# Optimization experiments

Hardware: AMD Instinct MI355X
Metric: run time of the kernel (lower is better)

The kernel has to match this reference:

```python
import jax, jax.numpy as jnp
import numpy as np

N_ATOMS = 512
N_SAMPLES = 2 ** 15  # 32768
N_ITER = 64


def time_domain_to_real(x):
    # rfft then concat(real, imag) along last dim -> length 2*(N//2+1)
    s = jnp.fft.rfft(x, axis=-1)
    return jnp.concatenate([s.real, s.imag], axis=-1)


def real_to_time_domain(x):
    half = x.shape[-1] // 2
    c = x[..., :half] + 1j * x[..., half:]
    return jnp.fft.irfft(c, axis=-1)  # n = 2*(half-1) = N_SAMPLES


def setup_inputs() -> dict:
    key = jax.random.key(0)
    k1, k2 = jax.random.split(key)
    x = jax.random.normal(k1, (64, 1, N_SAMPLES), dtype=jnp.float32)
    # learned atoms, initialized exactly as in Model.__init__
    env = jnp.linspace(1.0, 0.0, N_SAMPLES, dtype=jnp.float32) ** 12
    atoms_td = jax.random.uniform(k2, (1, N_ATOMS, N_SAMPLES), dtype=jnp.float32,
                                  minval=-0.01, maxval=0.01) * env[None, None, :]
    atoms = time_domain_to_real(atoms_td)  # (1, N_ATOMS, 32770)
    return {"x": x, "atoms": atoms}


def reference(x, atoms):
    xr = time_domain_to_real(x)            # (B, 1, L), L = 32770
    an = atoms / jnp.linalg.norm(atoms, axis=-1, keepdims=True)  # unit_norm over last axis
    an = an[0]                             # (A, L)
    res0 = xr[:, 0, :]                     # (B, L)
    rec0 = jnp.zeros_like(res0)

    def step(carry, _):
        res, rec = carry
        # sum(atoms * residual, -1) == dot products -> avoid (B,A,L) intermediate
        dots = jnp.einsum('bl,al->ba', res, an)      # (B, A)
        idx = jnp.argmax(dots, axis=1)               # (B,)
        best = an[idx] * res                         # take_along_dim(corr) == atoms[idx]*res
        return (res - best, rec + best), None

    (res, rec), _ = jax.lax.scan(step, (res0, rec0), None, length=N_ITER)
    reconstruction = real_to_time_domain(rec[:, None, :])  # (B, 1, N_SAMPLES)
    return reconstruction, res[:, None, :]
```

## Files before the change

kernel.cpp:

```cpp
#include <hip/hip_runtime.h>
#include <math.h>

#define NSAMP 32768
#define MH    16384
#define LFREQ 32770
#define NRE   16385
#define NB    64
#define NA    512
#define NITER 64
#define RSTR  32772

#define KPS    33280
#define NSL    64
#define USLICE 8
#define NCH    4097

typedef __attribute__((ext_vector_type(8))) short bf16x8;
typedef __attribute__((ext_vector_type(8))) unsigned short u16x8;
typedef __attribute__((ext_vector_type(4))) float f32x4;

__device__ __forceinline__ int rev4_14(int v) {
  unsigned r = __brev((unsigned)v) >> 18;
  r = ((r & 0x1555u) << 1) | ((r >> 1) & 0x1555u);
  return (int)r;
}

__device__ __forceinline__ unsigned short f2bf(float f) {
  unsigned u = __float_as_uint(f);
  u = (u + 0x7fffu + ((u >> 16) & 1u)) >> 16;
  return (unsigned short)u;
}
__device__ __forceinline__ float bf2f(unsigned short h) {
  return __uint_as_float(((unsigned)h) << 16);
}

__device__ __forceinline__ float2 cmul(float2 a, float2 b) {
  return make_float2(a.x * b.x - a.y * b.y, a.x * b.y + a.y * b.x);
}

__global__ __launch_bounds__(1024) void fft_fwd_kernel(const float* __restrict__ x,
                                                       float* __restrict__ res0,
                                                       unsigned short* __restrict__ resH,
                                                       unsigned short* __restrict__ resL) {
  extern __shared__ float2 s[];
  const int b = blockIdx.x, t = threadIdx.x;
  const float2* xrow = (const float2*)(x + (size_t)b * NSAMP);
  for (int m = t; m < MH; m += 1024) s[m] = xrow[rev4_14(m)];
  __syncthreads();
  for (int st = 0; st < 7; ++st) {
    const int q = 1 << (2 * st);
    const float fac = 6.283185307179586f / (float)(4 * q);
    for (int j = t; j < MH / 4; j += 1024) {
      const int blk = j >> (2 * st), pos = j & (q - 1);
      const int i0 = (blk << (2 * st + 2)) + pos;
      float sn, cs; __sincosf(fac * (float)pos, &sn, &cs);
      const float2 w1 = make_float2(cs, -sn);
      const float2 w2 = cmul(w1, w1);
      const float2 w3 = cmul(w2, w1);
      const float2 a0 = s[i0], a1 = s[i0 + q], a2 = s[i0 + 2 * q], a3 = s[i0 + 3 * q];
      const float2 x1 = cmul(w1, a1), x2 = cmul(w2, a2), x3 = cmul(w3, a3);
      const float2 s0 = make_float2(a0.x + x2.x, a0.y + x2.y);
      const float2 s1 = make_float2(a0.x - x2.x, a0.y - x2.y);
      const float2 t0 = make_float2(x1.x + x3.x, x1.y + x3.y);
      const float2 t1 = make_float2(x1.x - x3.x, x1.y - x3.y);
      s[i0]         = make_float2(s0.x + t0.x, s0.y + t0.y);
      s[i0 + q]     = make_float2(s1.x + t1.y, s1.y - t1.x);
      s[i0 + 2 * q] = make_float2(s0.x - t0.x, s0.y - t0.y);
      s[i0 + 3 * q] = make_float2(s1.x - t1.y, s1.y + t1.x);
    }
    __syncthreads();
  }
  float* rr = res0 + (size_t)b * RSTR;
  unsigned short* hrow = resH + (size_t)b * KPS;
  unsigned short* lrow = resL + (size_t)b * KPS;
  const float fac2 = 6.283185307179586f / (float)NSAMP;
  for (int k = t; k < MH; k += 1024) {
    if (k == 0) {
      const float2 z0 = s[0];
      const float dc = z0.x + z0.y, ny = z0.x - z0.y;
      rr[0] = dc;   rr[NRE] = 0.f;
      rr[MH] = ny;  rr[NRE + MH] = 0.f;
      unsigned short h;
      h = f2bf(dc); hrow[0] = h;  lrow[0] = f2bf(dc - bf2f(h));
      h = f2bf(ny); hrow[MH] = h; lrow[MH] = f2bf(ny - bf2f(h));
      hrow[NRE] = 0; lrow[NRE] = 0;
      hrow[NRE + MH] = 0; lrow[NRE + MH] = 0;
    } else {
      const float2 zk = s[k], zm = s[MH - k];
      const float xer = 0.5f * (zk.x + zm.x), xei = 0.5f * (zk.y - zm.y);
      const float p = 0.5f * (zk.y + zm.y);
      const float q = -0.5f * (zk.x - zm.x);
      float sn, cs; __sincosf(fac2 * (float)k, &sn, &cs);
      const float vr = xer + cs * p + sn * q;
      const float vi = xei + cs * q - sn * p;
      rr[k]       = vr;
      rr[NRE + k] = vi;
      unsigned short h;
      h = f2bf(vr); hrow[k] = h;       lrow[k] = f2bf(vr - bf2f(h));
      h = f2bf(vi); hrow[NRE + k] = h; lrow[NRE + k] = f2bf(vi - bf2f(h));
    }
  }
}

__global__ __launch_bounds__(1024) void fft_inv_kernel(const float* __restrict__ rec,
                                                       float* __restrict__ out) {
  extern __shared__ float2 s[];
  const int b = blockIdx.x, t = threadIdx.x;
  const float* rr = rec + (size_t)b * RSTR;
  const float fac2 = 6.283185307179586f / (float)NSAMP;
  for (int m = t; m < MH; m += 1024) {
    const int k = rev4_14(m);
    float2 z;
    if (k == 0) {
      const float a0 = rr[0], aM = rr[MH];
      z = make_float2(0.5f * (a0 + aM), 0.5f * (a0 - aM));
    } else {
      const float xr_ = rr[k],       xi_ = rr[NRE + k];
      const float mr  = rr[MH - k],  mi  = rr[NRE + MH - k];
      const float xer = 0.5f * (xr_ + mr), xei = 0.5f * (xi_ - mi);
      const float er  = 0.5f * (xr_ - mr), ei  = 0.5f * (xi_ + mi);
      float sn, cs; __sincosf(fac2 * (float)k, &sn, &cs);
      const float xor_ = cs * er - sn * ei;
      const float xoi  = cs * ei + sn * er;
      z = make_float2(xer - xoi, xei + xor_);
    }
    s[m] = z;
  }
  __syncthreads();
  for (int st = 0; st < 7; ++st) {
    const int q = 1 << (2 * st);
    const float fac = 6.283185307179586f / (float)(4 * q);
    for (int j = t; j < MH / 4; j += 1024) {
      const int blk = j >> (2 * st), pos = j & (q - 1);
      const int i0 = (blk << (2 * st + 2)) + pos;
      float sn, cs; __sincosf(fac * (float)pos, &sn, &cs);
      const float2 w1 = make_float2(cs, sn);
      const float2 w2 = cmul(w1, w1);
      const float2 w3 = cmul(w2, w1);
      const float2 a0 = s[i0], a1 = s[i0 + q], a2 = s[i0 + 2 * q], a3 = s[i0 + 3 * q];
      const float2 x1 = cmul(w1, a1), x2 = cmul(w2, a2), x3 = cmul(w3, a3);
      const float2 s0 = make_float2(a0.x + x2.x, a0.y + x2.y);
      const float2 s1 = make_float2(a0.x - x2.x, a0.y - x2.y);
      const float2 t0 = make_float2(x1.x + x3.x, x1.y + x3.y);
      const float2 t1 = make_float2(x1.x - x3.x, x1.y - x3.y);
      s[i0]         = make_float2(s0.x + t0.x, s0.y + t0.y);
      s[i0 + q]     = make_float2(s1.x - t1.y, s1.y + t1.x);
      s[i0 + 2 * q] = make_float2(s0.x - t0.x, s0.y - t0.y);
      s[i0 + 3 * q] = make_float2(s1.x + t1.y, s1.y - t1.x);
    }
    __syncthreads();
  }
  const float inv = 1.0f / (float)MH;
  float2* orow = (float2*)(out + (size_t)b * NSAMP);
  for (int m = t; m < MH; m += 1024) {
    const float2 z = s[m];
    orow[m] = make_float2(z.x * inv, z.y * inv);
  }
}

__global__ __launch_bounds__(256) void atom_norm_kernel(const float* __restrict__ atoms,
                                                        float* __restrict__ rnorm,
                                                        float* __restrict__ anv) {
  const int a = blockIdx.x, t = threadIdx.x;
  const float2* row2 = (const float2*)(atoms + (size_t)a * LFREQ);
  float ss = 0.f;
  for (int i = t; i < LFREQ / 2; i += 256) {
    const float2 v = row2[i];
    ss += v.x * v.x + v.y * v.y;
  }
  __shared__ float red[256];
  red[t] = ss; __syncthreads();
  for (int st = 128; st > 0; st >>= 1) {
    if (t < st) red[t] += red[t + st];
    __syncthreads();
  }
  if (t == 0) {
    const float rn = 1.0f / sqrtf(red[0]);
    rnorm[a] = rn;
    anv[a] = atoms[(size_t)a * LFREQ + 32768] * rn;
  }
}

__global__ __launch_bounds__(256) void an_bf16_kernel(const float* __restrict__ atoms,
                                                      const float* __restrict__ rnorm,
                                                      unsigned short* __restrict__ anH,
                                                      unsigned short* __restrict__ anL) {
  const int quarter = blockIdx.x;
  const int a = blockIdx.y;
  const int t = threadIdx.x;
  const float rn = rnorm[a];
  const float* row = atoms + (size_t)a * LFREQ;
  unsigned short* hrow = anH + (size_t)a * KPS;
  unsigned short* lrow = anL + (size_t)a * KPS;
  const int c0 = quarter * 1040;
  const int c1 = min(c0 + 1040, KPS / 8);
  for (int c = c0 + t; c < c1; c += 256) {
    const int k0 = c * 8;
    float v[8];
    if (k0 + 8 <= LFREQ) {
      #pragma unroll
      for (int e = 0; e < 4; ++e) {
        const float2 p = *(const float2*)(row + k0 + 2 * e);
        v[2 * e] = p.x; v[2 * e + 1] = p.y;
      }
    } else {
      #pragma unroll
      for (int e = 0; e < 8; ++e) v[e] = (k0 + e < LFREQ) ? row[k0 + e] : 0.f;
    }
    u16x8 hv, lv;
    #pragma unroll
    for (int e = 0; e < 8; ++e) {
      const float sv = v[e] * rn;
      const unsigned short h = f2bf(sv);
      hv[e] = h;
      lv[e] = f2bf(sv - bf2f(h));
    }
    *(u16x8*)(hrow + k0) = hv;
    *(u16x8*)(lrow + k0) = lv;
  }
}

__global__ __launch_bounds__(256) void dots_mfma_kernel(const unsigned short* __restrict__ resH,
                                                        const unsigned short* __restrict__ resL,
                                                        const unsigned short* __restrict__ anH,
                                                        const unsigned short* __restrict__ anL,
                                                        float* __restrict__ partials) {
  __shared__ char smem[65536];
  const int slice = blockIdx.x;
  const int atile = blockIdx.y;
  const int t = threadIdx.x;
  const int w = t >> 6, l = t & 63;
  const int bh = w >> 1, ah = w & 1;
  const int kc0 = slice * 512;

  const unsigned short* gtab = (w == 0) ? resH : (w == 1) ? resL : (w == 2) ? anH : anL;
  const int rowoff = (w >= 2) ? atile * 64 : 0;
  const int lrow = rowoff + (l & 15);
  const int lkof = (l >> 4) * 8;

  f32x4 acc00 = {0.f,0.f,0.f,0.f}, acc01 = acc00, acc10 = acc00, acc11 = acc00;

#define STAGE(cc, bb)                                                                     \
  {                                                                                       \
    const int kc = kc0 + (cc) * 64;                                                       \
    _Pragma("unroll")                                                                     \
    for (int si = 0; si < 8; ++si) {                                                      \
      const unsigned short* g = gtab + (size_t)(lrow + (si >> 1) * 16) * KPS              \
                                + kc + (si & 1) * 32 + lkof;                              \
      char* d = smem + (bb) * 32768 + w * 8192 + si * 1024;                               \
      __builtin_amdgcn_global_load_lds((const __attribute__((address_space(1))) void*)g,  \
                                       (__attribute__((address_space(3))) void*)d,        \
                                       16, 0, 0);                                         \
    }                                                                                     \
  }

#define COMPUTE(bb)                                                                      \
  {                                                                                       \
    const char* base = smem + (bb) * 32768;                                               \
    _Pragma("unroll")                                                                     \
    for (int kk = 0; kk < 2; ++kk) {                                                      \
      const bf16x8 aH0 = *(const bf16x8*)(base + ((bh * 2 + 0) * 2 + kk) * 1024 + l * 16);\
      const bf16x8 aH1 = *(const bf16x8*)(base + ((bh * 2 + 1) * 2 + kk) * 1024 + l * 16);\
      const bf16x8 aL0 = *(const bf16x8*)(base + 8192 + ((bh * 2 + 0) * 2 + kk) * 1024 + l * 16);\
      const bf16x8 aL1 = *(const bf16x8*)(base + 8192 + ((bh * 2 + 1) * 2 + kk) * 1024 + l * 16);\
      const bf16x8 bH0 = *(const bf16x8*)(base + 16384 + ((ah * 2 + 0) * 2 + kk) * 1024 + l * 16);\
      const bf16x8 bH1 = *(const bf16x8*)(base + 16384 + ((ah * 2 + 1) * 2 + kk) * 1024 + l * 16);\
      const bf16x8 bL0 = *(const bf16x8*)(base + 24576 + ((ah * 2 + 0) * 2 + kk) * 1024 + l * 16);\
      const bf16x8 bL1 = *(const bf16x8*)(base + 24576 + ((ah * 2 + 1) * 2 + kk) * 1024 + l * 16);\
      acc00 = __builtin_amdgcn_mfma_f32_16x16x32_bf16(aH0, bH0, acc00, 0, 0, 0);          \
      acc01 = __builtin_amdgcn_mfma_f32_16x16x32_bf16(aH0, bH1, acc01, 0, 0, 0);          \
      acc10 = __builtin_amdgcn_mfma_f32_16x16x32_bf16(aH1, bH0, acc10, 0, 0, 0);          \
      acc11 = __builtin_amdgcn_mfma_f32_16x16x32_bf16(aH1, bH1, acc11, 0, 0, 0);          \
      acc00 = __builtin_amdgcn_mfma_f32_16x16x32_bf16(aH0, bL0, acc00, 0, 0, 0);          \
      acc01 = __builtin_amdgcn_mfma_f32_16x16x32_bf16(aH0, bL1, acc01, 0, 0, 0);          \
      acc10 = __builtin_amdgcn_mfma_f32_16x16x32_bf16(aH1, bL0, acc10, 0, 0, 0);          \
      acc11 = __builtin_amdgcn_mfma_f32_16x16x32_bf16(aH1, bL1, acc11, 0, 0, 0);          \
      acc00 = __builtin_amdgcn_mfma_f32_16x16x32_bf16(aL0, bH0, acc00, 0, 0, 0);          \
      acc01 = __builtin_amdgcn_mfma_f32_16x16x32_bf16(aL0, bH1, acc01, 0, 0, 0);          \
      acc10 = __builtin_amdgcn_mfma_f32_16x16x32_bf16(aL1, bH0, acc10, 0, 0, 0);          \
      acc11 = __builtin_amdgcn_mfma_f32_16x16x32_bf16(aL1, bH1, acc11, 0, 0, 0);          \
    }                                                                                     \
  }

  STAGE(0, 0);
  #pragma unroll
  for (int c = 0; c < 8; ++c) {
    const int buf = c & 1;
    if (c < 7) {
      STAGE(c + 1, buf ^ 1);
      asm volatile("s_waitcnt vmcnt(8)" ::: "memory");
    } else {
      asm volatile("s_waitcnt vmcnt(0)" ::: "memory");
    }
    __builtin_amdgcn_s_barrier();
    __builtin_amdgcn_sched_barrier(0);
    COMPUTE(buf);
    __builtin_amdgcn_sched_barrier(0);
    __builtin_amdgcn_s_barrier();
  }
#undef STAGE
#undef COMPUTE

  const int brow = bh * 32 + (l >> 4) * 4;
  const int acol = atile * 64 + ah * 32 + (l & 15);
  float* pp = partials + ((size_t)brow * NSL + slice) * NA + acol;
  const size_t bstr = (size_t)NSL * NA;
  #pragma unroll
  for (int e = 0; e < 4; ++e) {
    pp[(size_t)e * bstr]             = acc00[e];
    pp[(size_t)e * bstr + 16]        = acc01[e];
    pp[(size_t)(16 + e) * bstr]      = acc10[e];
    pp[(size_t)(16 + e) * bstr + 16] = acc11[e];
  }
}

__global__ __launch_bounds__(256) void reduce_argmax_kernel(const float* __restrict__ partials,
                                                            const unsigned short* __restrict__ resH,
                                                            const unsigned short* __restrict__ resL,
                                                            const float* __restrict__ anv,
                                                            int* __restrict__ bestidx) {
  const int b = blockIdx.x, t = threadIdx.x;
  const float* pb = partials + (size_t)b * NSL * NA;
  float d0 = 0.f, d1 = 0.f;
  #pragma unroll 16
  for (int s = 0; s < NSL; ++s) {
    d0 += pb[(size_t)s * NA + t];
    d1 += pb[(size_t)s * NA + t + 256];
  }
  const float rv = bf2f(resH[(size_t)b * KPS + 32768]) +
                   bf2f(resL[(size_t)b * KPS + 32768]);
  d0 = fmaf(rv, anv[t], d0);
  d1 = fmaf(rv, anv[t + 256], d1);
  float best = d0; int bi = t;
  if (d1 > best) { best = d1; bi = t + 256; }
  __shared__ float sv[256]; __shared__ int si[256];
  sv[t] = best; si[t] = bi; __syncthreads();
  for (int st = 128; st > 0; st >>= 1) {
    if (t < st) {
      const float v2 = sv[t + st]; const int i2 = si[t + st];
      if (v2 > sv[t] || (v2 == sv[t] && i2 < si[t])) { sv[t] = v2; si[t] = i2; }
    }
    __syncthreads();
  }
  if (t == 0) bestidx[b] = si[0];
}

__global__ __launch_bounds__(256) void update_kernel(const float* __restrict__ atoms,
                                                     const float* __restrict__ rnorm,
                                                     const int* __restrict__ bestidx,
                                                     unsigned short* __restrict__ resH,
                                                     unsigned short* __restrict__ resL,
                                                     const float* __restrict__ res0,
                                                     float* __restrict__ rec,
                                                     float* __restrict__ out2,
                                                     int final_out) {
  const int slice = blockIdx.x;
  const int b = blockIdx.y;
  const int t = threadIdx.x;
  const int idx = bestidx[b];
  const float rn = rnorm[idx];
  const float* arow = atoms + (size_t)idx * LFREQ;
  unsigned short* hrow = resH + (size_t)b * KPS;
  unsigned short* lrow = resL + (size_t)b * KPS;
  const float* r0row = res0 + (size_t)b * RSTR;
  float* recrow = rec + (size_t)b * RSTR;
  float* orow = out2 + (size_t)b * LFREQ;
  const int c0 = slice * 513;
  const int c1 = min(c0 + 513, NCH);
  for (int c = c0 + t; c < c1; c += 256) {
    const int k0 = c * 8;
    if (k0 + 8 <= LFREQ) {
      const u16x8 hv0 = *(const u16x8*)(hrow + k0);
      const u16x8 lv0 = *(const u16x8*)(lrow + k0);
      float av[8];
      #pragma unroll
      for (int e = 0; e < 4; ++e) {
        const float2 p = *(const float2*)(arow + k0 + 2 * e);
        av[2 * e] = p.x; av[2 * e + 1] = p.y;
      }
      float nv[8];
      u16x8 hv, lv;
      #pragma unroll
      for (int e = 0; e < 8; ++e) {
        const float r = bf2f(hv0[e]) + bf2f(lv0[e]);
        const float bx = av[e] * rn * r;
        nv[e] = r - bx;
        const unsigned short h = f2bf(nv[e]);
        hv[e] = h;
        lv[e] = f2bf(nv[e] - bf2f(h));
      }
      *(u16x8*)(hrow + k0) = hv;
      *(u16x8*)(lrow + k0) = lv;
      if (final_out) {
        #pragma unroll
        for (int e = 0; e < 2; ++e) {
          const float4 r0 = *(const float4*)(r0row + k0 + 4 * e);
          *(float4*)(orow + k0 + 4 * e) = make_float4(nv[4*e], nv[4*e+1], nv[4*e+2], nv[4*e+3]);
          *(float4*)(recrow + k0 + 4 * e) = make_float4(r0.x - nv[4*e], r0.y - nv[4*e+1],
                                                       r0.z - nv[4*e+2], r0.w - nv[4*e+3]);
        }
      }
    } else {
      for (int e = 0; e < 8; ++e) {
        const int k = k0 + e;
        if (k < LFREQ) {
          const float r = bf2f(hrow[k]) + bf2f(lrow[k]);
          const float bx = arow[k] * rn * r;
          const float nx = r - bx;
          const unsigned short h = f2bf(nx);
          hrow[k] = h;
          lrow[k] = f2bf(nx - bf2f(h));
          if (final_out) {
            orow[k] = nx;
            recrow[k] = r0row[k] - nx;
          }
        }
      }
    }
  }
}

extern "C" void kernel_launch(void* const* d_in, const int* in_sizes, int n_in,
                              void* d_out, int out_size, void* d_ws, size_t ws_size,
                              hipStream_t stream) {
  const float* x = (const float*)d_in[0];
  const float* atoms = (const float*)d_in[1];
  float* out = (float*)d_out;

  float* res0 = (float*)d_ws;
  float* rec = res0 + (size_t)NB * RSTR;
  float* rnorm = rec + (size_t)NB * RSTR;
  float* anv = rnorm + NA;
  float* partials = anv + NA;
  int* bestidx = (int*)(partials + (size_t)NB * NSL * NA);
  unsigned short* resH = (unsigned short*)(bestidx + 64);
  unsigned short* resL = resH + (size_t)NB * KPS;
  unsigned short* anH  = resL + (size_t)NB * KPS;
  unsigned short* anL  = anH + (size_t)NA * KPS;

  hipMemsetAsync(resH, 0, (size_t)NB * KPS * sizeof(unsigned short) * 2, stream);
  atom_norm_kernel<<<NA, 256, 0, stream>>>(atoms, rnorm, anv);
  an_bf16_kernel<<<dim3(4, NA), 256, 0, stream>>>(atoms, rnorm, anH, anL);
  fft_fwd_kernel<<<NB, 1024, MH * sizeof(float2), stream>>>(x, res0, resH, resL);

  float* res_out = out + (size_t)NB * NSAMP;
  for (int it = 0; it < NITER; ++it) {
    dots_mfma_kernel<<<dim3(NSL, 8), 256, 0, stream>>>(resH, resL, anH, anL, partials);
    reduce_argmax_kernel<<<NB, 256, 0, stream>>>(partials, resH, resL, anv, bestidx);
    update_kernel<<<dim3(USLICE, NB), 256, 0, stream>>>(atoms, rnorm, bestidx,
                                                        resH, resL, res0, rec, res_out,
                                                        (it == NITER - 1) ? 1 : 0);
  }

  fft_inv_kernel<<<NB, 1024, MH * sizeof(float2), stream>>>(rec, out);
}
```

Baseline: 2.008 ms.

## Fuse argmax reduction into update kernel and widen dots tile to 128 atoms

The dots MFMA kernel now uses 512 threads per block, and each block covers 128 atoms instead of 64. This halves the grid's y dimension and shares each staged residual tile across twice as many atoms. The separate reduce/argmax kernel is removed: every update block redoes the partial-sum reduction and argmax for its batch row, which drops one launch per iteration and the bestidx round trip. The cost is that all 8 slices repeat the same reduction work, and the LDS footprint grows to 96KB. The resH/resL memset is also dropped, which risks leaving the padding region uninitialized.

```diff
diff --git a/kernel.cpp b/kernel.cpp
--- a/kernel.cpp
+++ b/kernel.cpp
@@ -12,6 +12,7 @@
 
 #define KPS    33280
 #define NSL    64
+#define BN2    128
 #define USLICE 8
 #define NCH    4097
 
@@ -220,23 +221,18 @@
   }
 }
 
-__global__ __launch_bounds__(256) void dots_mfma_kernel(const unsigned short* __restrict__ resH,
+__global__ __launch_bounds__(512) void dots_mfma_kernel(const unsigned short* __restrict__ resH,
                                                         const unsigned short* __restrict__ resL,
                                                         const unsigned short* __restrict__ anH,
                                                         const unsigned short* __restrict__ anL,
                                                         float* __restrict__ partials) {
-  __shared__ char smem[65536];
+  __shared__ char smem[98304];
   const int slice = blockIdx.x;
   const int atile = blockIdx.y;
   const int t = threadIdx.x;
   const int w = t >> 6, l = t & 63;
-  const int bh = w >> 1, ah = w & 1;
+  const int bh = w >> 2, aq = w & 3;
   const int kc0 = slice * 512;
-
-  const unsigned short* gtab = (w == 0) ? resH : (w == 1) ? resL : (w == 2) ? anH : anL;
-  const int rowoff = (w >= 2) ? atile * 64 : 0;
-  const int lrow = rowoff + (l & 15);
-  const int lkof = (l >> 4) * 8;
 
   f32x4 acc00 = {0.f,0.f,0.f,0.f}, acc01 = acc00, acc10 = acc00, acc11 = acc00;
 
@@ -244,10 +240,16 @@
   {                                                                                       \
     const int kc = kc0 + (cc) * 64;                                                       \
     _Pragma("unroll")                                                                     \
-    for (int si = 0; si < 8; ++si) {                                                      \
-      const unsigned short* g = gtab + (size_t)(lrow + (si >> 1) * 16) * KPS              \
-                                + kc + (si & 1) * 32 + lkof;                              \
-      char* d = smem + (bb) * 32768 + w * 8192 + si * 1024;                               \
+    for (int j = 0; j < 6; ++j) {                                                         \
+      const int u = w * 6 + j;                                                            \
+      const unsigned short* gt = (u < 8) ? resH : (u < 16) ? resL : (u < 32) ? anH : anL; \
+      const int base = (u < 8) ? 0 : (u < 16) ? 8192 : (u < 32) ? 16384 : 32768;          \
+      const int usec = u - ((u < 8) ? 0 : (u < 16) ? 8 : (u < 32) ? 16 : 32);             \
+      const int row0 = (u < 16) ? 0 : atile * BN2;                                        \
+      const int rt = usec >> 1, kk = usec & 1;                                            \
+      const unsigned short* g = gt + (size_t)(row0 + rt * 16 + (l & 15)) * KPS            \
+                                + kc + kk * 32 + (l >> 4) * 8;                            \
+      char* d = smem + (bb) * 49152 + base + usec * 1024 + l * 16;                        \
       __builtin_amdgcn_global_load_lds((const __attribute__((address_space(1))) void*)g,  \
                                        (__attribute__((address_space(3))) void*)d,        \
                                        16, 0, 0);                                         \
@@ -256,17 +258,17 @@
 
 #define COMPUTE(bb)                                                                      \
   {                                                                                       \
-    const char* base = smem + (bb) * 32768;                                               \
+    const char* base = smem + (bb) * 49152;                                               \
     _Pragma("unroll")                                                                     \
     for (int kk = 0; kk < 2; ++kk) {                                                      \
       const bf16x8 aH0 = *(const bf16x8*)(base + ((bh * 2 + 0) * 2 + kk) * 1024 + l * 16);\
       const bf16x8 aH1 = *(const bf16x8*)(base + ((bh * 2 + 1) * 2 + kk) * 1024 + l * 16);\
       const bf16x8 aL0 = *(const bf16x8*)(base + 8192 + ((bh * 2 + 0) * 2 + kk) * 1024 + l * 16);\
       const bf16x8 aL1 = *(const bf16x8*)(base + 8192 + ((bh * 2 + 1) * 2 + kk) * 1024 + l * 16);\
-      const bf16x8 bH0 = *(const bf16x8*)(base + 16384 + ((ah * 2 + 0) * 2 + kk) * 1024 + l * 16);\
-      const bf16x8 bH1 = *(const bf16x8*)(base + 16384 + ((ah * 2 + 1) * 2 + kk) * 1024 + l * 16);\
-      const bf16x8 bL0 = *(const bf16x8*)(base + 24576 + ((ah * 2 + 0) * 2 + kk) * 1024 + l * 16);\
-      const bf16x8 bL1 = *(const bf16x8*)(base + 24576 + ((ah * 2 + 1) * 2 + kk) * 1024 + l * 16);\
+      const bf16x8 bH0 = *(const bf16x8*)(base + 16384 + ((aq * 2 + 0) * 2 + kk) * 1024 + l * 16);\
+      const bf16x8 bH1 = *(const bf16x8*)(base + 16384 + ((aq * 2 + 1) * 2 + kk) * 1024 + l * 16);\
+      const bf16x8 bL0 = *(const bf16x8*)(base + 32768 + ((aq * 2 + 0) * 2 + kk) * 1024 + l * 16);\
+      const bf16x8 bL1 = *(const bf16x8*)(base + 32768 + ((aq * 2 + 1) * 2 + kk) * 1024 + l * 16);\
       acc00 = __builtin_amdgcn_mfma_f32_16x16x32_bf16(aH0, bH0, acc00, 0, 0, 0);          \
       acc01 = __builtin_amdgcn_mfma_f32_16x16x32_bf16(aH0, bH1, acc01, 0, 0, 0);          \
       acc10 = __builtin_amdgcn_mfma_f32_16x16x32_bf16(aH1, bH0, acc10, 0, 0, 0);          \
@@ -288,7 +290,7 @@
     const int buf = c & 1;
     if (c < 7) {
       STAGE(c + 1, buf ^ 1);
-      asm volatile("s_waitcnt vmcnt(8)" ::: "memory");
+      asm volatile("s_waitcnt vmcnt(6)" ::: "memory");
     } else {
       asm volatile("s_waitcnt vmcnt(0)" ::: "memory");
     }
@@ -301,25 +303,34 @@
 #undef STAGE
 #undef COMPUTE
 
-  const int brow = bh * 32 + (l >> 4) * 4;
-  const int acol = atile * 64 + ah * 32 + (l & 15);
-  float* pp = partials + ((size_t)brow * NSL + slice) * NA + acol;
+  const int acol = atile * BN2 + aq * 32 + (l & 15);
   const size_t bstr = (size_t)NSL * NA;
   #pragma unroll
   for (int e = 0; e < 4; ++e) {
-    pp[(size_t)e * bstr]             = acc00[e];
-    pp[(size_t)e * bstr + 16]        = acc01[e];
-    pp[(size_t)(16 + e) * bstr]      = acc10[e];
-    pp[(size_t)(16 + e) * bstr + 16] = acc11[e];
-  }
-}
-
-__global__ __launch_bounds__(256) void reduce_argmax_kernel(const float* __restrict__ partials,
-                                                            const unsigned short* __restrict__ resH,
-                                                            const unsigned short* __restrict__ resL,
-                                                            const float* __restrict__ anv,
-                                                            int* __restrict__ bestidx) {
-  const int b = blockIdx.x, t = threadIdx.x;
+    const size_t r0 = (size_t)(bh * 32 + (l >> 4) * 4 + e);
+    partials[r0 * bstr + (size_t)slice * NA + acol]             = acc00[e];
+    partials[r0 * bstr + (size_t)slice * NA + acol + 16]        = acc01[e];
+    partials[(r0 + 16) * bstr + (size_t)slice * NA + acol]      = acc10[e];
+    partials[(r0 + 16) * bstr + (size_t)slice * NA + acol + 16] = acc11[e];
+  }
+}
+
+__global__ __launch_bounds__(256) void update_kernel(const float* __restrict__ atoms,
+                                                     const float* __restrict__ rnorm,
+                                                     const float* __restrict__ partials,
+                                                     const float* __restrict__ anv,
+                                                     unsigned short* __restrict__ resH,
+                                                     unsigned short* __restrict__ resL,
+                                                     const float* __restrict__ res0,
+                                                     float* __restrict__ rec,
+                                                     float* __restrict__ out2,
+                                                     int final_out) {
+  const int slice = blockIdx.x;
+  const int b = blockIdx.y;
+  const int t = threadIdx.x;
+  unsigned short* hrow = resH + (size_t)b * KPS;
+  unsigned short* lrow = resL + (size_t)b * KPS;
+
   const float* pb = partials + (size_t)b * NSL * NA;
   float d0 = 0.f, d1 = 0.f;
   #pragma unroll 16
@@ -327,8 +338,7 @@
     d0 += pb[(size_t)s * NA + t];
     d1 += pb[(size_t)s * NA + t + 256];
   }
-  const float rv = bf2f(resH[(size_t)b * KPS + 32768]) +
-                   bf2f(resL[(size_t)b * KPS + 32768]);
+  const float rv = bf2f(hrow[32768]) + bf2f(lrow[32768]);
   d0 = fmaf(rv, anv[t], d0);
   d1 = fmaf(rv, anv[t + 256], d1);
   float best = d0; int bi = t;
@@ -342,26 +352,9 @@
     }
     __syncthreads();
   }
-  if (t == 0) bestidx[b] = si[0];
-}
-
-__global__ __launch_bounds__(256) void update_kernel(const float* __restrict__ atoms,
-                                                     const float* __restrict__ rnorm,
-                                                     const int* __restrict__ bestidx,
-                                                     unsigned short* __restrict__ resH,
-                                                     unsigned short* __restrict__ resL,
-                                                     const float* __restrict__ res0,
-                                                     float* __restrict__ rec,
-                                                     float* __restrict__ out2,
-                                                     int final_out) {
-  const int slice = blockIdx.x;
-  const int b = blockIdx.y;
-  const int t = threadIdx.x;
-  const int idx = bestidx[b];
+  const int idx = si[0];
   const float rn = rnorm[idx];
   const float* arow = atoms + (size_t)idx * LFREQ;
-  unsigned short* hrow = resH + (size_t)b * KPS;
-  unsigned short* lrow = resL + (size_t)b * KPS;
   const float* r0row = res0 + (size_t)b * RSTR;
   float* recrow = rec + (size_t)b * RSTR;
   float* orow = out2 + (size_t)b * LFREQ;
@@ -432,22 +425,19 @@
   float* rnorm = rec + (size_t)NB * RSTR;
   float* anv = rnorm + NA;
   float* partials = anv + NA;
-  int* bestidx = (int*)(partials + (size_t)NB * NSL * NA);
-  unsigned short* resH = (unsigned short*)(bestidx + 64);
+  unsigned short* resH = (unsigned short*)(partials + (size_t)NB * NSL * NA);
   unsigned short* resL = resH + (size_t)NB * KPS;
   unsigned short* anH  = resL + (size_t)NB * KPS;
   unsigned short* anL  = anH + (size_t)NA * KPS;
 
-  hipMemsetAsync(resH, 0, (size_t)NB * KPS * sizeof(unsigned short) * 2, stream);
   atom_norm_kernel<<<NA, 256, 0, stream>>>(atoms, rnorm, anv);
   an_bf16_kernel<<<dim3(4, NA), 256, 0, stream>>>(atoms, rnorm, anH, anL);
   fft_fwd_kernel<<<NB, 1024, MH * sizeof(float2), stream>>>(x, res0, resH, resL);
 
   float* res_out = out + (size_t)NB * NSAMP;
   for (int it = 0; it < NITER; ++it) {
-    dots_mfma_kernel<<<dim3(NSL, 8), 256, 0, stream>>>(resH, resL, anH, anL, partials);
-    reduce_argmax_kernel<<<NB, 256, 0, stream>>>(partials, resH, resL, anv, bestidx);
-    update_kernel<<<dim3(USLICE, NB), 256, 0, stream>>>(atoms, rnorm, bestidx,
+    dots_mfma_kernel<<<dim3(NSL, 4), 512, 0, stream>>>(resH, resL, anH, anL, partials);
+    update_kernel<<<dim3(USLICE, NB), 256, 0, stream>>>(atoms, rnorm, partials, anv,
                                                         resH, resL, res0, rec, res_out,
                                                         (it == NITER - 1) ? 1 : 0);
   }
```

Result: slower. 2.086 ms (+3.9%).
